# Kernel optimization log

Hardware: AMD Instinct MI355X
Metric: run time of the kernel (lower is better)

Reference implementation:

```python
import jax, jax.numpy as jnp
import numpy as np
import math

B, S, D, H, L, F = 32, 512, 512, 8, 4, 2048
DK = D // H
EPS = 1e-5


def _cosine_pos_emb(seq_len, d_model):
    pe = np.zeros((seq_len, d_model), dtype=np.float32)
    position = np.arange(seq_len, dtype=np.float32)[:, None]
    div_term = np.exp(np.arange(0, d_model, 2, dtype=np.float32) * (-math.log(10000.0) / d_model))
    pe[:, 0::2] = np.sin(position * div_term)
    pe[:, 1::2] = np.cos(position * div_term)
    return jnp.asarray(pe[None])  # (1, S, D)


def setup_inputs() -> dict:
    key = jax.random.key(0)
    ks = jax.random.split(key, 12)
    w = 0.02
    return {
        "q_embed_data": jax.random.normal(ks[0], (B, S, D), jnp.float32),
        "qa_embed_data": jax.random.normal(ks[1], (B, S, D), jnp.float32),
        "forget_rate": jax.random.uniform(ks[2], (B, S, 1), jnp.float32),
        "pos_emb": _cosine_pos_emb(S, D),
        # per-layer stacked params (torch Linear convention: W is (out,in))
        "Wk": w * jax.random.normal(ks[3], (L, D, D), jnp.float32),
        "bk": jnp.zeros((L, D), jnp.float32),
        "Wv": w * jax.random.normal(ks[4], (L, D, D), jnp.float32),
        "bv": jnp.zeros((L, D), jnp.float32),
        "Wo": w * jax.random.normal(ks[5], (L, D, D), jnp.float32),
        "bo": jnp.zeros((L, D), jnp.float32),
        "W1": w * jax.random.normal(ks[6], (L, F, D), jnp.float32),
        "b1": jnp.zeros((L, F), jnp.float32),
        "W2": w * jax.random.normal(ks[7], (L, D, F), jnp.float32),
        "b2": jnp.zeros((L, D), jnp.float32),
        "ln1_g": jnp.ones((L, D), jnp.float32),
        "ln1_b": jnp.zeros((L, D), jnp.float32),
        "ln2_g": jnp.ones((L, D), jnp.float32),
        "ln2_b": jnp.zeros((L, D), jnp.float32),
    }


def _layer_norm(x, g, b):
    mu = jnp.mean(x, axis=-1, keepdims=True)
    var = jnp.mean(jnp.square(x - mu), axis=-1, keepdims=True)
    return (x - mu) * jax.lax.rsqrt(var + EPS) * g + b


def _forward(q_embed_data, qa_embed_data, forget_rate, pos_emb,
             Wk, bk, Wv, bv, Wo, bo, W1, b1, W2, b2,
             ln1_g, ln1_b, ln2_g, ln2_b):
    x = q_embed_data + pos_emb   # queries/keys stream
    y = qa_embed_data + pos_emb  # values stream (fixed across layers)
    scale = 1.0 / math.sqrt(DK)
    # mask=0 path: triu(k=0)==0 -> strictly past positions only (j < i)
    allowed = jnp.tril(jnp.ones((S, S), dtype=bool), k=-1)
    fr = forget_rate[:, None, :, :]  # (B,1,S,1): row-wise decay on scores
    neg = jnp.asarray(-1e32, x.dtype)

    def block(x, p):
        wk, bk_, wv, bv_, wo, bo_, w1, b1_, w2, b2_, g1, be1, g2, be2 = p
        # kq_same=1: q and k share the k_linear projection (so q == k here)
        kq = (jnp.einsum('bsd,ed->bse', x, wk) + bk_).reshape(B, S, H, DK).transpose(0, 2, 1, 3)
        v = (jnp.einsum('bsd,ed->bse', y, wv) + bv_).reshape(B, S, H, DK).transpose(0, 2, 1, 3)
        scores = jnp.einsum('bhsd,bhtd->bhst', kq, kq) * scale
        scores = scores * fr
        scores = jnp.where(allowed, scores, neg)
        attn = jax.nn.softmax(scores, axis=-1)
        attn = attn.at[:, :, 0, :].set(0.0)  # zero_pad: first query row zeroed
        ctx = jnp.einsum('bhst,bhtd->bhsd', attn, v).transpose(0, 2, 1, 3).reshape(B, S, D)
        out = jnp.einsum('bsd,ed->bse', ctx, wo) + bo_
        x = _layer_norm(x + out, g1, be1)
        ff = jnp.einsum('bsf,df->bsd', jax.nn.relu(jnp.einsum('bsd,fd->bsf', x, w1) + b1_), w2) + b2_
        x = _layer_norm(x + ff, g2, be2)
        return x, None

    x, _ = jax.lax.scan(block, x, (Wk, bk, Wv, bv, Wo, bo, W1, b1, W2, b2, ln1_g, ln1_b, ln2_g, ln2_b))
    return x


def reference(q_embed_data, qa_embed_data, forget_rate, pos_emb,
              Wk, bk, Wv, bv, Wo, bo, W1, b1, W2, b2,
              ln1_g, ln1_b, ln2_g, ln2_b):
    return _forward(q_embed_data, qa_embed_data, forget_rate, pos_emb,
                    Wk, bk, Wv, bv, Wo, bo, W1, b1, W2, b2,
                    ln1_g, ln1_b, ln2_g, ln2_b)
```

## Files before the change

### kernel.cpp

```cpp
#include <hip/hip_runtime.h>
#include <hip/hip_bf16.h>

constexpr int B_ = 32, S_ = 512, D_ = 512, H_ = 8, L_ = 4, F_ = 2048, DK_ = 64;

typedef __attribute__((ext_vector_type(8))) short short8;
typedef __attribute__((ext_vector_type(4))) float f32x4;

__device__ inline unsigned short f2b(float f) {
  union { __hip_bfloat16 h; unsigned short u; } cv;
  cv.h = __float2bfloat16(f);
  return cv.u;
}
__device__ inline float b2f(unsigned short u) {
  union { unsigned int i; float f; } c;
  c.i = ((unsigned int)u) << 16;
  return c.f;
}
__device__ inline float waveReduceSum(float v) {
  #pragma unroll
  for (int o = 32; o > 0; o >>= 1) v += __shfl_xor(v, o);
  return v;
}

__global__ void prep_kernel(const float4* __restrict__ q, const float4* __restrict__ qa,
                            const float4* __restrict__ pos, float4* __restrict__ xf,
                            uint2* __restrict__ xb, uint2* __restrict__ yb) {
  int i = blockIdx.x * blockDim.x + threadIdx.x;
  float4 p = pos[i & 65535];
  float4 a = q[i], c = qa[i];
  float4 xv, yv;
  xv.x = a.x + p.x; xv.y = a.y + p.y; xv.z = a.z + p.z; xv.w = a.w + p.w;
  yv.x = c.x + p.x; yv.y = c.y + p.y; yv.z = c.z + p.z; yv.w = c.w + p.w;
  xf[i] = xv;
  uint2 px, py;
  px.x = (unsigned)f2b(xv.x) | ((unsigned)f2b(xv.y) << 16);
  px.y = (unsigned)f2b(xv.z) | ((unsigned)f2b(xv.w) << 16);
  py.x = (unsigned)f2b(yv.x) | ((unsigned)f2b(yv.y) << 16);
  py.y = (unsigned)f2b(yv.z) | ((unsigned)f2b(yv.w) << 16);
  xb[i] = px;
  yb[i] = py;
}

__global__ void cast_kernel(const float4* __restrict__ src, uint2* __restrict__ dst, int n4) {
  int i = blockIdx.x * blockDim.x + threadIdx.x;
  if (i >= n4) return;
  float4 v = src[i];
  uint2 p;
  p.x = (unsigned)f2b(v.x) | ((unsigned)f2b(v.y) << 16);
  p.y = (unsigned)f2b(v.z) | ((unsigned)f2b(v.w) << 16);
  dst[i] = p;
}

template<int BM, int RELU, int STORE>
__global__ __launch_bounds__(512, 2) void gemm256_kernel(
    const __hip_bfloat16* __restrict__ A,
    const __hip_bfloat16* __restrict__ W,
    const float* __restrict__ bias,
    const __hip_bfloat16* __restrict__ A2,
    const __hip_bfloat16* __restrict__ W2,
    const float* __restrict__ bias2,
    __hip_bfloat16* __restrict__ Cb,
    __hip_bfloat16* __restrict__ Cb2,
    int Ndim, int Kdim, int kLen)
{
  constexpr int ABUF = BM * 64;
  constexpr int WREG = 4 * ABUF;
  constexpr int M_REP = BM / 32;
  constexpr int LPT = BM / 128 + 2;
  __shared__ char lds[WREG + 65536];
  const int tid = threadIdx.x, wave = tid >> 6, lane = tid & 63;
  const int rl = lane & 15, gq = lane >> 4;
  const int wr = wave >> 2, wc = wave & 3;

  const int nwg = gridDim.x * gridDim.y;
  const int lin = blockIdx.y * gridDim.x + blockIdx.x;
  const int swz = (lin & 7) * (nwg >> 3) + (lin >> 3);
  const int bx = swz % gridDim.x, by = swz / gridDim.x;

  const int row0 = by * BM;
  const int col0 = bx * 256;

  const __hip_bfloat16* Ap = A;
  const __hip_bfloat16* Wp = W;
  const float* bp = bias;
  int kOff = blockIdx.z * kLen;
  if (STORE == 3) {
    kOff = 0;
    if (blockIdx.z) { Ap = A2; Wp = W2; bp = bias2; }
  }

  f32x4 acc[M_REP][4] = {};
  const int ntiles = kLen >> 5;

  auto stage = [&](int kt) {
    const int buf = kt & 3;
    const int kbase = kOff + (kt << 5);
    #pragma unroll
    for (int r = 0; r < BM / 128; ++r) {
      int p = r * 8192 + tid * 16;
      int R = p >> 6, c = (p >> 4) & 3;
      int gc = c ^ ((R >> 1) & 3);
      const __hip_bfloat16* src = Ap + (size_t)(row0 + R) * Kdim + kbase + gc * 8;
      __builtin_amdgcn_global_load_lds(
          (const __attribute__((address_space(1))) void*)src,
          (__attribute__((address_space(3))) void*)(lds + buf * ABUF + p), 16, 0, 0);
    }
    #pragma unroll
    for (int r = 0; r < 2; ++r) {
      int p = r * 8192 + tid * 16;
      int R = p >> 6, c = (p >> 4) & 3;
      int gc = c ^ ((R >> 1) & 3);
      const __hip_bfloat16* src = Wp + (size_t)(col0 + R) * Kdim + kbase + gc * 8;
      __builtin_amdgcn_global_load_lds(
          (const __attribute__((address_space(1))) void*)src,
          (__attribute__((address_space(3))) void*)(lds + WREG + buf * 16384 + p), 16, 0, 0);
    }
  };

  stage(0); stage(1); stage(2);
  for (int kt = 0; kt < ntiles; ++kt) {
    if (kt + 2 < ntiles) {
      asm volatile("s_waitcnt vmcnt(%0)" :: "n"(2 * LPT) : "memory");
    } else if (kt + 1 < ntiles) {
      asm volatile("s_waitcnt vmcnt(%0)" :: "n"(LPT) : "memory");
    } else {
      asm volatile("s_waitcnt vmcnt(0)" ::: "memory");
    }
    __builtin_amdgcn_sched_barrier(0);
    __builtin_amdgcn_s_barrier();
    __builtin_amdgcn_sched_barrier(0);
    if (kt + 3 < ntiles) stage(kt + 3);

    const int abase = (kt & 3) * ABUF;
    const int wbase = WREG + (kt & 3) * 16384;
    short8 bF[4];
    #pragma unroll
    for (int n = 0; n < 4; ++n) {
      int rr = wc * 64 + n * 16 + rl;
      bF[n] = *(const short8*)(lds + wbase + rr * 64 + ((gq ^ ((rr >> 1) & 3)) << 4));
    }
    short8 aF[M_REP];
    #pragma unroll
    for (int m = 0; m < M_REP; ++m) {
      int rr = wr * (BM / 2) + m * 16 + rl;
      aF[m] = *(const short8*)(lds + abase + rr * 64 + ((gq ^ ((rr >> 1) & 3)) << 4));
    }
    __builtin_amdgcn_s_setprio(1);
    #pragma unroll
    for (int m = 0; m < M_REP; ++m)
      #pragma unroll
      for (int n = 0; n < 4; ++n)
        acc[m][n] = __builtin_amdgcn_mfma_f32_16x16x32_bf16(aF[m], bF[n], acc[m][n], 0, 0, 0);
    __builtin_amdgcn_s_setprio(0);
  }

  __syncthreads();
  char* sw = lds + wave * (BM * 64);
  const bool vt = (STORE == 2) || (STORE == 3 && blockIdx.z == 1);
  const bool addb = (STORE == 3) ? true : ((bias != nullptr) && (blockIdx.z == 0));
  float bvv[4];
  #pragma unroll
  for (int n = 0; n < 4; ++n)
    bvv[n] = addb ? bp[col0 + wc * 64 + n * 16 + rl] : 0.0f;

  #pragma unroll
  for (int n = 0; n < 4; ++n)
    #pragma unroll
    for (int m = 0; m < M_REP; ++m)
      #pragma unroll
      for (int j = 0; j < 4; ++j) {
        float val = acc[m][n][j] + bvv[n];
        if (RELU) val = fmaxf(val, 0.0f);
        int addr;
        if (vt) {
          int orow = n * 16 + rl, ocol = m * 16 + gq * 4 + j;
          addr = orow * 128 + ((ocol * 2) ^ ((orow & 7) << 4));
        } else {
          int orow = m * 16 + gq * 4 + j;
          addr = orow * 128 + (((n * 16 + rl) * 2) ^ (((orow >> 1) & 7) << 4));
        }
        *(unsigned short*)(sw + addr) = f2b(val);
      }
  asm volatile("s_waitcnt lgkmcnt(0)" ::: "memory");
  __builtin_amdgcn_sched_barrier(0);

  __hip_bfloat16* Cbd = blockIdx.z ? Cb2 : Cb;
  const int cchunk = lane & 7;
  if (vt) {
    const int bh64 = ((row0 >> 9) * 8 + (col0 >> 6) + wc) * 64;
    const int tbase = (row0 & 511) + wr * 64;
    #pragma unroll
    for (int it = 0; it < 8; ++it) {
      int d0 = it * 8 + (lane >> 3);
      uint4 vv = *(const uint4*)(sw + d0 * 128 + ((cchunk * 16) ^ ((d0 & 7) << 4)));
      *(uint4*)((char*)Cbd + ((size_t)(bh64 + d0) * 512 + tbase) * 2 + cchunk * 16) = vv;
    }
  } else {
    #pragma unroll
    for (int it = 0; it < BM / 16; ++it) {
      int orow = it * 8 + (lane >> 3);
      uint4 vv = *(const uint4*)(sw + orow * 128 + ((cchunk * 16) ^ (((orow >> 1) & 7) << 4)));
      *(uint4*)((char*)Cbd + ((size_t)(row0 + wr * (BM / 2) + orow) * Ndim + col0 + wc * 64) * 2 +
                cchunk * 16) = vv;
    }
  }
}

__global__ __launch_bounds__(256, 2) void fattn_kernel(
    const __hip_bfloat16* __restrict__ kq,
    const __hip_bfloat16* __restrict__ vT,
    const float* __restrict__ fr,
    __hip_bfloat16* __restrict__ ctx)
{
  __shared__ char lds[40960];
  const int tid = threadIdx.x, wave = tid >> 6, lane = tid & 63;
  const int rl = lane & 15, gq = lane >> 4;
  const int lin = blockIdx.x;
  const int qb = (3 - (lin >> 8)) * 128;
  const int wpi = lin & 255;
  const int bh = (wpi & 7) * 32 + (wpi >> 3);
  const int b = bh >> 3, h = bh & 7;
  const size_t kqbase = ((size_t)b * S_) * D_ + h * DK_;
  const size_t vtbase = ((size_t)bh * DK_) * S_;
  const int qw0 = qb + wave * 32;
  const int qw_end = qw0 + 32;

  short8 qA[2][2];
  #pragma unroll
  for (int qf = 0; qf < 2; ++qf)
    #pragma unroll
    for (int kf = 0; kf < 2; ++kf)
      qA[qf][kf] = *(const short8*)(kq + kqbase + (size_t)(qw0 + qf * 16 + rl) * D_ + kf * 32 + gq * 8);

  float sfv[2][4];
  #pragma unroll
  for (int qf = 0; qf < 2; ++qf)
    #pragma unroll
    for (int j = 0; j < 4; ++j)
      sfv[qf][j] = fr[b * S_ + qw0 + qf * 16 + gq * 4 + j] * 0.125f;

  f32x4 o[2][4] = {};
  float mrow[2][4], lrow[2][4];
  #pragma unroll
  for (int qf = 0; qf < 2; ++qf)
    #pragma unroll
    for (int j = 0; j < 4; ++j) { mrow[qf][j] = -3.0e38f; lrow[qf][j] = 0.0f; }

  int sgoff[2], sldsoff[2];
  #pragma unroll
  for (int c = 0; c < 2; ++c) {
    int p = (wave * 2 + c) * 1024 + lane * 16;
    int r = p >> 7;
    int ch = (p >> 4) & 7;
    sgoff[c] = r * 1024 + ((ch ^ (r & 7)) << 4);
    sldsoff[c] = (wave * 2 + c) * 1024;
  }
  const char* kgbase = (const char*)kq + kqbase * 2;
  const char* vgbase = (const char*)vT + vtbase * 2;

  auto stage = [&](int ti, int d) {
    const int t0 = ti << 6;
    #pragma unroll
    for (int c = 0; c < 2; ++c) {
      __builtin_amdgcn_global_load_lds(
          (const __attribute__((address_space(1))) void*)(kgbase + (size_t)t0 * 1024 + sgoff[c]),
          (__attribute__((address_space(3))) void*)(lds + d * 8192 + sldsoff[c]), 16, 0, 0);
      __builtin_amdgcn_global_load_lds(
          (const __attribute__((address_space(1))) void*)(vgbase + t0 * 2 + sgoff[c]),
          (__attribute__((address_space(3))) void*)(lds + 16384 + d * 8192 + sldsoff[c]), 16, 0, 0);
    }
  };

  const int nt = (qb + 128) >> 6;
  stage(0, 0);
  for (int ti = 0; ti < nt; ++ti) {
    const int t0 = ti << 6;
    const int d = ti & 1;
    if (ti + 1 < nt) {
      stage(ti + 1, d ^ 1);
      asm volatile("s_waitcnt vmcnt(4)" ::: "memory");
    } else {
      asm volatile("s_waitcnt vmcnt(0)" ::: "memory");
    }
    __builtin_amdgcn_sched_barrier(0);
    __builtin_amdgcn_s_barrier();
    __builtin_amdgcn_sched_barrier(0);

    if (t0 < qw_end) {
      short8 kB[4][2];
      #pragma unroll
      for (int tf = 0; tf < 4; ++tf)
        #pragma unroll
        for (int kf = 0; kf < 2; ++kf) {
          int r = tf * 16 + rl;
          kB[tf][kf] = *(const short8*)(lds + d * 8192 + r * 128 + (((kf * 4 + gq) ^ (r & 7)) << 4));
        }
      short8 vB[4][2];
      #pragma unroll
      for (int df = 0; df < 4; ++df)
        #pragma unroll
        for (int kf = 0; kf < 2; ++kf) {
          int r = df * 16 + rl;
          vB[df][kf] = *(const short8*)(lds + 16384 + d * 8192 + r * 128 + (((kf * 4 + gq) ^ (r & 7)) << 4));
        }

      #pragma unroll
      for (int qf = 0; qf < 2; ++qf) {
        f32x4 c4[4] = {};
        #pragma unroll
        for (int tf = 0; tf < 4; ++tf)
          #pragma unroll
          for (int kf = 0; kf < 2; ++kf)
            c4[tf] = __builtin_amdgcn_mfma_f32_16x16x32_bf16(qA[qf][kf], kB[tf][kf], c4[tf], 0, 0, 0);

        const int qg0 = qw0 + qf * 16 + gq * 4;
        #pragma unroll
        for (int tf = 0; tf < 4; ++tf) {
          int tg = t0 + tf * 16 + rl;
          #pragma unroll
          for (int j = 0; j < 4; ++j) {
            float s = c4[tf][j] * sfv[qf][j];
            c4[tf][j] = (tg >= qg0 + j) ? -3.0e38f : s;
          }
        }
        float tm[4];
        #pragma unroll
        for (int j = 0; j < 4; ++j) {
          tm[j] = fmaxf(fmaxf(c4[0][j], c4[1][j]), fmaxf(c4[2][j], c4[3][j]));
          #pragma unroll
          for (int msk = 1; msk < 16; msk <<= 1) tm[j] = fmaxf(tm[j], __shfl_xor(tm[j], msk));
        }
        #pragma unroll
        for (int j = 0; j < 4; ++j) {
          float mn = fmaxf(mrow[qf][j], tm[j]);
          float fac = __expf(mrow[qf][j] - mn);
          mrow[qf][j] = mn;
          lrow[qf][j] *= fac;
          #pragma unroll
          for (int df = 0; df < 4; ++df) o[qf][df][j] *= fac;
        }
        float rs[4] = {0.f, 0.f, 0.f, 0.f};
        #pragma unroll
        for (int tf = 0; tf < 4; ++tf) {
          int tloc = tf * 16 + rl;
          #pragma unroll
          for (int j = 0; j < 4; ++j) {
            float e = __expf(c4[tf][j] - mrow[qf][j]);
            rs[j] += e;
            int qloc = gq * 4 + j;
            int addr = 32768 + wave * 2048 + qloc * 128 +
                       ((((tloc >> 3) ^ (qloc & 7)) << 4)) + (tloc & 7) * 2;
            *(unsigned short*)(lds + addr) = f2b(e);
          }
        }
        #pragma unroll
        for (int j = 0; j < 4; ++j) {
          float r = rs[j];
          #pragma unroll
          for (int msk = 1; msk < 16; msk <<= 1) r += __shfl_xor(r, msk);
          lrow[qf][j] += r;
        }
        asm volatile("s_waitcnt lgkmcnt(0)" ::: "memory");
        __builtin_amdgcn_sched_barrier(0);
        short8 pA[2];
        #pragma unroll
        for (int kf = 0; kf < 2; ++kf)
          pA[kf] = *(const short8*)(lds + 32768 + wave * 2048 + rl * 128 +
                                    (((kf * 4 + gq) ^ (rl & 7)) << 4));
        #pragma unroll
        for (int df = 0; df < 4; ++df)
          #pragma unroll
          for (int kf = 0; kf < 2; ++kf)
            o[qf][df] = __builtin_amdgcn_mfma_f32_16x16x32_bf16(pA[kf], vB[df][kf], o[qf][df], 0, 0, 0);
      }
    }
    __builtin_amdgcn_sched_barrier(0);
    __builtin_amdgcn_s_barrier();
    __builtin_amdgcn_sched_barrier(0);
  }

  #pragma unroll
  for (int qf = 0; qf < 2; ++qf)
    #pragma unroll
    for (int j = 0; j < 4; ++j) {
      int qg = qw0 + qf * 16 + gq * 4 + j;
      float inv = (qg == 0) ? 0.0f : 1.0f / lrow[qf][j];
      #pragma unroll
      for (int df = 0; df < 4; ++df) {
        union { __hip_bfloat16 hh; unsigned short u; } cv;
        cv.u = f2b(o[qf][df][j] * inv);
        ctx[((size_t)(b * S_ + qg)) * D_ + h * DK_ + df * 16 + rl] = cv.hh;
      }
    }
}

template<int NADD>
__global__ __launch_bounds__(256) void ln_kernel(
    const float4* __restrict__ xin, const uint4* __restrict__ add,
    const uint4* __restrict__ add2,
    const float* __restrict__ g, const float* __restrict__ bta,
    float4* xf_out, uint2* __restrict__ xb_out)
{
  const int lane = threadIdx.x & 63, wv = threadIdx.x >> 6;
  const size_t row = (size_t)blockIdx.x * 4 + wv;
  const size_t base4 = row * 128;

  float4 x0 = xin[base4 + lane * 2], x1 = xin[base4 + lane * 2 + 1];
  uint4 ab = add[row * 64 + lane];
  const unsigned short* ap = (const unsigned short*)&ab;
  float v[8];
  v[0] = x0.x; v[1] = x0.y; v[2] = x0.z; v[3] = x0.w;
  v[4] = x1.x; v[5] = x1.y; v[6] = x1.z; v[7] = x1.w;
  #pragma unroll
  for (int i = 0; i < 8; ++i) v[i] += b2f(ap[i]);
  if (NADD == 2) {
    uint4 ab2 = add2[row * 64 + lane];
    const unsigned short* ap2 = (const unsigned short*)&ab2;
    #pragma unroll
    for (int i = 0; i < 8; ++i) v[i] += b2f(ap2[i]);
  }
  float s = 0.0f;
  #pragma unroll
  for (int i = 0; i < 8; ++i) s += v[i];
  s = waveReduceSum(s);
  float mu = s * (1.0f / 512.0f);
  float vs = 0.0f;
  #pragma unroll
  for (int i = 0; i < 8; ++i) { float dd = v[i] - mu; vs += dd * dd; }
  vs = waveReduceSum(vs);
  float rstd = rsqrtf(vs * (1.0f / 512.0f) + 1e-5f);

  const int c0i = lane * 8;
  float4 gg0 = *(const float4*)(g + c0i), gg1 = *(const float4*)(g + c0i + 4);
  float4 bb0 = *(const float4*)(bta + c0i), bb1 = *(const float4*)(bta + c0i + 4);
  float o[8];
  o[0] = (v[0] - mu) * rstd * gg0.x + bb0.x;
  o[1] = (v[1] - mu) * rstd * gg0.y + bb0.y;
  o[2] = (v[2] - mu) * rstd * gg0.z + bb0.z;
  o[3] = (v[3] - mu) * rstd * gg0.w + bb0.w;
  o[4] = (v[4] - mu) * rstd * gg1.x + bb1.x;
  o[5] = (v[5] - mu) * rstd * gg1.y + bb1.y;
  o[6] = (v[6] - mu) * rstd * gg1.z + bb1.z;
  o[7] = (v[7] - mu) * rstd * gg1.w + bb1.w;
  float4 w0, w1;
  w0.x = o[0]; w0.y = o[1]; w0.z = o[2]; w0.w = o[3];
  w1.x = o[4]; w1.y = o[5]; w1.z = o[6]; w1.w = o[7];
  xf_out[base4 + lane * 2] = w0;
  xf_out[base4 + lane * 2 + 1] = w1;
  uint2 p0, p1;
  p0.x = (unsigned)f2b(o[0]) | ((unsigned)f2b(o[1]) << 16);
  p0.y = (unsigned)f2b(o[2]) | ((unsigned)f2b(o[3]) << 16);
  p1.x = (unsigned)f2b(o[4]) | ((unsigned)f2b(o[5]) << 16);
  p1.y = (unsigned)f2b(o[6]) | ((unsigned)f2b(o[7]) << 16);
  xb_out[row * 128 + lane * 2] = p0;
  xb_out[row * 128 + lane * 2 + 1] = p1;
}

extern "C" void kernel_launch(void* const* d_in, const int* in_sizes, int n_in,
                              void* d_out, int out_size, void* d_ws, size_t ws_size,
                              hipStream_t stream) {
  (void)in_sizes; (void)n_in; (void)out_size; (void)ws_size;
  const float* q   = (const float*)d_in[0];
  const float* qa  = (const float*)d_in[1];
  const float* frr = (const float*)d_in[2];
  const float* pos = (const float*)d_in[3];
  const float* Wk  = (const float*)d_in[4];
  const float* bk  = (const float*)d_in[5];
  const float* Wv  = (const float*)d_in[6];
  const float* bv  = (const float*)d_in[7];
  const float* Wo  = (const float*)d_in[8];
  const float* bo  = (const float*)d_in[9];
  const float* W1  = (const float*)d_in[10];
  const float* b1  = (const float*)d_in[11];
  const float* W2  = (const float*)d_in[12];
  const float* b2  = (const float*)d_in[13];
  const float* g1  = (const float*)d_in[14];
  const float* be1 = (const float*)d_in[15];
  const float* g2  = (const float*)d_in[16];
  const float* be2 = (const float*)d_in[17];

  char* ws = (char*)d_ws;
  float*          xf   = (float*)(ws + 0);
  __hip_bfloat16* xb   = (__hip_bfloat16*)(ws + 33554432);
  __hip_bfloat16* yb   = (__hip_bfloat16*)(ws + 50331648);
  __hip_bfloat16* kqb  = (__hip_bfloat16*)(ws + 67108864);
  __hip_bfloat16* vtb  = (__hip_bfloat16*)(ws + 83886080);
  __hip_bfloat16* ctxb = (__hip_bfloat16*)(ws + 100663296);
  __hip_bfloat16* hb   = (__hip_bfloat16*)(ws + 117440512);
  __hip_bfloat16* wkb  = (__hip_bfloat16*)(ws + 184549376);
  __hip_bfloat16* wvb  = (__hip_bfloat16*)(ws + 186646528);
  __hip_bfloat16* wob  = (__hip_bfloat16*)(ws + 188743680);
  __hip_bfloat16* w1b  = (__hip_bfloat16*)(ws + 190840832);
  __hip_bfloat16* w2b  = (__hip_bfloat16*)(ws + 199229440);
  __hip_bfloat16* obf = (__hip_bfloat16*)(ws + 67108864);
  __hip_bfloat16* pf0 = (__hip_bfloat16*)(ws + 83886080);
  __hip_bfloat16* pf1 = (__hip_bfloat16*)(ws + 100663296);

  prep_kernel<<<8192, 256, 0, stream>>>((const float4*)q, (const float4*)qa,
                                        (const float4*)pos, (float4*)xf,
                                        (uint2*)xb, (uint2*)yb);
  cast_kernel<<<1024, 256, 0, stream>>>((const float4*)Wk, (uint2*)wkb, 262144);
  cast_kernel<<<1024, 256, 0, stream>>>((const float4*)Wv, (uint2*)wvb, 262144);
  cast_kernel<<<1024, 256, 0, stream>>>((const float4*)Wo, (uint2*)wob, 262144);
  cast_kernel<<<4096, 256, 0, stream>>>((const float4*)W1, (uint2*)w1b, 1048576);
  cast_kernel<<<4096, 256, 0, stream>>>((const float4*)W2, (uint2*)w2b, 1048576);

  for (int l = 0; l < L_; ++l) {
    gemm256_kernel<128,0,3><<<dim3(2, 128, 2), 512, 0, stream>>>(
        xb, wkb + (size_t)l * 262144, bk + l * 512,
        yb, wvb + (size_t)l * 262144, bv + l * 512,
        kqb, vtb, 512, 512, 512);
    fattn_kernel<<<1024, 256, 0, stream>>>(kqb, vtb, frr, ctxb);
    gemm256_kernel<128,0,0><<<dim3(2, 128, 1), 512, 0, stream>>>(
        ctxb, wob + (size_t)l * 262144, bo + l * 512,
        nullptr, nullptr, nullptr, obf, nullptr, 512, 512, 512);
    ln_kernel<1><<<4096, 256, 0, stream>>>((const float4*)xf, (const uint4*)obf, nullptr,
                                           g1 + l * 512, be1 + l * 512,
                                           (float4*)xf, (uint2*)xb);
    gemm256_kernel<256,1,0><<<dim3(8, 64, 1), 512, 0, stream>>>(
        xb, w1b + (size_t)l * 1048576, b1 + l * 2048,
        nullptr, nullptr, nullptr, hb, nullptr, 2048, 512, 512);
    gemm256_kernel<256,0,0><<<dim3(2, 64, 2), 512, 0, stream>>>(
        hb, w2b + (size_t)l * 1048576, b2 + l * 512,
        nullptr, nullptr, nullptr, pf0, pf1, 512, 2048, 1024);
    float* lnout = (l == L_ - 1) ? (float*)d_out : xf;
    ln_kernel<2><<<4096, 256, 0, stream>>>((const float4*)xf, (const uint4*)pf0,
                                           (const uint4*)pf1,
                                           g2 + l * 512, be2 + l * 512,
                                           (float4*)lnout, (uint2*)xb);
  }
}
```

Baseline: 836.9 us.

## Replace 256-wide 4-stage GEMM with 128x128 double-buffered GEMM

The GEMM kernel moves from 512-thread blocks with 128/256x256 tiles and a 4-deep async LDS pipeline to 256-thread blocks with 128x128 tiles and simple double buffering synchronised by a block barrier each k-step. Launch grids grow to match. The intent is to raise the number of workgroups and lower LDS use per block for better occupancy. In exchange, data reuse per tile drops and the shallower prefetch with a full barrier per iteration exposes more memory latency.

```diff
diff --git a/kernel.cpp b/kernel.cpp
--- a/kernel.cpp
+++ b/kernel.cpp
@@ -51,8 +51,8 @@
   dst[i] = p;
 }
 
-template<int BM, int RELU, int STORE>
-__global__ __launch_bounds__(512, 2) void gemm256_kernel(
+template<int RELU, int STORE>
+__global__ __launch_bounds__(256, 2) void gemm128_kernel(
     const __hip_bfloat16* __restrict__ A,
     const __hip_bfloat16* __restrict__ W,
     const float* __restrict__ bias,
@@ -63,22 +63,18 @@
     __hip_bfloat16* __restrict__ Cb2,
     int Ndim, int Kdim, int kLen)
 {
-  constexpr int ABUF = BM * 64;
-  constexpr int WREG = 4 * ABUF;
-  constexpr int M_REP = BM / 32;
-  constexpr int LPT = BM / 128 + 2;
-  __shared__ char lds[WREG + 65536];
+  __shared__ char lds[32768];
   const int tid = threadIdx.x, wave = tid >> 6, lane = tid & 63;
   const int rl = lane & 15, gq = lane >> 4;
-  const int wr = wave >> 2, wc = wave & 3;
+  const int wr = wave >> 1, wc = wave & 1;
 
   const int nwg = gridDim.x * gridDim.y;
   const int lin = blockIdx.y * gridDim.x + blockIdx.x;
   const int swz = (lin & 7) * (nwg >> 3) + (lin >> 3);
   const int bx = swz % gridDim.x, by = swz / gridDim.x;
 
-  const int row0 = by * BM;
-  const int col0 = bx * 256;
+  const int row0 = by * 128;
+  const int col0 = bx * 128;
 
   const __hip_bfloat16* Ap = A;
   const __hip_bfloat16* Wp = W;
@@ -89,74 +85,56 @@
     if (blockIdx.z) { Ap = A2; Wp = W2; bp = bias2; }
   }
 
-  f32x4 acc[M_REP][4] = {};
+  f32x4 acc[4][4] = {};
   const int ntiles = kLen >> 5;
 
-  auto stage = [&](int kt) {
-    const int buf = kt & 3;
+  auto stage = [&](int kt, int d) {
     const int kbase = kOff + (kt << 5);
     #pragma unroll
-    for (int r = 0; r < BM / 128; ++r) {
-      int p = r * 8192 + tid * 16;
+    for (int r = 0; r < 2; ++r) {
+      int p = r * 4096 + tid * 16;
       int R = p >> 6, c = (p >> 4) & 3;
       int gc = c ^ ((R >> 1) & 3);
-      const __hip_bfloat16* src = Ap + (size_t)(row0 + R) * Kdim + kbase + gc * 8;
+      const __hip_bfloat16* srcA = Ap + (size_t)(row0 + R) * Kdim + kbase + gc * 8;
       __builtin_amdgcn_global_load_lds(
-          (const __attribute__((address_space(1))) void*)src,
-          (__attribute__((address_space(3))) void*)(lds + buf * ABUF + p), 16, 0, 0);
-    }
-    #pragma unroll
-    for (int r = 0; r < 2; ++r) {
-      int p = r * 8192 + tid * 16;
-      int R = p >> 6, c = (p >> 4) & 3;
-      int gc = c ^ ((R >> 1) & 3);
-      const __hip_bfloat16* src = Wp + (size_t)(col0 + R) * Kdim + kbase + gc * 8;
+          (const __attribute__((address_space(1))) void*)srcA,
+          (__attribute__((address_space(3))) void*)(lds + d * 8192 + p), 16, 0, 0);
+      const __hip_bfloat16* srcW = Wp + (size_t)(col0 + R) * Kdim + kbase + gc * 8;
       __builtin_amdgcn_global_load_lds(
-          (const __attribute__((address_space(1))) void*)src,
-          (__attribute__((address_space(3))) void*)(lds + WREG + buf * 16384 + p), 16, 0, 0);
+          (const __attribute__((address_space(1))) void*)srcW,
+          (__attribute__((address_space(3))) void*)(lds + 16384 + d * 8192 + p), 16, 0, 0);
     }
   };
 
-  stage(0); stage(1); stage(2);
+  stage(0, 0);
+  __syncthreads();
   for (int kt = 0; kt < ntiles; ++kt) {
-    if (kt + 2 < ntiles) {
-      asm volatile("s_waitcnt vmcnt(%0)" :: "n"(2 * LPT) : "memory");
-    } else if (kt + 1 < ntiles) {
-      asm volatile("s_waitcnt vmcnt(%0)" :: "n"(LPT) : "memory");
-    } else {
-      asm volatile("s_waitcnt vmcnt(0)" ::: "memory");
-    }
-    __builtin_amdgcn_sched_barrier(0);
-    __builtin_amdgcn_s_barrier();
-    __builtin_amdgcn_sched_barrier(0);
-    if (kt + 3 < ntiles) stage(kt + 3);
-
-    const int abase = (kt & 3) * ABUF;
-    const int wbase = WREG + (kt & 3) * 16384;
-    short8 bF[4];
+    const int d = kt & 1;
+    if (kt + 1 < ntiles) stage(kt + 1, d ^ 1);
+
+    short8 aF[4], bF[4];
+    #pragma unroll
+    for (int m = 0; m < 4; ++m) {
+      int rr = wr * 64 + m * 16 + rl;
+      aF[m] = *(const short8*)(lds + d * 8192 + rr * 64 + ((gq ^ ((rr >> 1) & 3)) << 4));
+    }
     #pragma unroll
     for (int n = 0; n < 4; ++n) {
       int rr = wc * 64 + n * 16 + rl;
-      bF[n] = *(const short8*)(lds + wbase + rr * 64 + ((gq ^ ((rr >> 1) & 3)) << 4));
-    }
-    short8 aF[M_REP];
-    #pragma unroll
-    for (int m = 0; m < M_REP; ++m) {
-      int rr = wr * (BM / 2) + m * 16 + rl;
-      aF[m] = *(const short8*)(lds + abase + rr * 64 + ((gq ^ ((rr >> 1) & 3)) << 4));
+      bF[n] = *(const short8*)(lds + 16384 + d * 8192 + rr * 64 + ((gq ^ ((rr >> 1) & 3)) << 4));
     }
     __builtin_amdgcn_s_setprio(1);
     #pragma unroll
-    for (int m = 0; m < M_REP; ++m)
+    for (int m = 0; m < 4; ++m)
       #pragma unroll
       for (int n = 0; n < 4; ++n)
         acc[m][n] = __builtin_amdgcn_mfma_f32_16x16x32_bf16(aF[m], bF[n], acc[m][n], 0, 0, 0);
     __builtin_amdgcn_s_setprio(0);
-  }
-
-  __syncthreads();
-  char* sw = lds + wave * (BM * 64);
-  const bool vt = (STORE == 2) || (STORE == 3 && blockIdx.z == 1);
+    __syncthreads();
+  }
+
+  char* sw = lds + wave * 8192;
+  const bool vt = (STORE == 3) && (blockIdx.z == 1);
   const bool addb = (STORE == 3) ? true : ((bias != nullptr) && (blockIdx.z == 0));
   float bvv[4];
   #pragma unroll
@@ -166,7 +144,7 @@
   #pragma unroll
   for (int n = 0; n < 4; ++n)
     #pragma unroll
-    for (int m = 0; m < M_REP; ++m)
+    for (int m = 0; m < 4; ++m)
       #pragma unroll
       for (int j = 0; j < 4; ++j) {
         float val = acc[m][n][j] + bvv[n];
@@ -197,10 +175,10 @@
     }
   } else {
     #pragma unroll
-    for (int it = 0; it < BM / 16; ++it) {
+    for (int it = 0; it < 8; ++it) {
       int orow = it * 8 + (lane >> 3);
       uint4 vv = *(const uint4*)(sw + orow * 128 + ((cchunk * 16) ^ (((orow >> 1) & 7) << 4)));
-      *(uint4*)((char*)Cbd + ((size_t)(row0 + wr * (BM / 2) + orow) * Ndim + col0 + wc * 64) * 2 +
+      *(uint4*)((char*)Cbd + ((size_t)(row0 + wr * 64 + orow) * Ndim + col0 + wc * 64) * 2 +
                 cchunk * 16) = vv;
     }
   }
@@ -506,21 +484,21 @@
   cast_kernel<<<4096, 256, 0, stream>>>((const float4*)W2, (uint2*)w2b, 1048576);
 
   for (int l = 0; l < L_; ++l) {
-    gemm256_kernel<128,0,3><<<dim3(2, 128, 2), 512, 0, stream>>>(
+    gemm128_kernel<0,3><<<dim3(4, 128, 2), 256, 0, stream>>>(
         xb, wkb + (size_t)l * 262144, bk + l * 512,
         yb, wvb + (size_t)l * 262144, bv + l * 512,
         kqb, vtb, 512, 512, 512);
     fattn_kernel<<<1024, 256, 0, stream>>>(kqb, vtb, frr, ctxb);
-    gemm256_kernel<128,0,0><<<dim3(2, 128, 1), 512, 0, stream>>>(
+    gemm128_kernel<0,0><<<dim3(4, 128, 1), 256, 0, stream>>>(
         ctxb, wob + (size_t)l * 262144, bo + l * 512,
         nullptr, nullptr, nullptr, obf, nullptr, 512, 512, 512);
     ln_kernel<1><<<4096, 256, 0, stream>>>((const float4*)xf, (const uint4*)obf, nullptr,
                                            g1 + l * 512, be1 + l * 512,
                                            (float4*)xf, (uint2*)xb);
-    gemm256_kernel<256,1,0><<<dim3(8, 64, 1), 512, 0, stream>>>(
+    gemm128_kernel<1,0><<<dim3(16, 128, 1), 256, 0, stream>>>(
         xb, w1b + (size_t)l * 1048576, b1 + l * 2048,
         nullptr, nullptr, nullptr, hb, nullptr, 2048, 512, 512);
-    gemm256_kernel<256,0,0><<<dim3(2, 64, 2), 512, 0, stream>>>(
+    gemm128_kernel<0,0><<<dim3(4, 128, 2), 256, 0, stream>>>(
         hb, w2b + (size_t)l * 1048576, b2 + l * 512,
         nullptr, nullptr, nullptr, pf0, pf1, 512, 2048, 1024);
     float* lnout = (l == L_ - 1) ? (float*)d_out : xf;
```

Result: no change. 848.6 us (+1.4%).
